# Kernel tuning notes

Hardware: AMD Instinct MI355X
Metric: run time of the kernel (lower is better)

Reference implementation:

```python
import jax, jax.numpy as jnp
import numpy as np

B = 16            # batch of graphs
N = 512           # n_node
D = 32            # embedding_dim
MAXN = 16         # max_neighbors
E = MAXN * (N - 1)   # 8176 edges per graph
SLEFT = N * D
FSS = 601         # full_support_size
NA = N - 1        # num_actions (so one-hot rows == B*n_node)
IN0 = D + 1       # sa feature dim
NTOT = B * N


def _gat(x, snd, rcv, W, a_src, a_dst, b):
    # single-head GATConv, add_self_loops=False
    h = x @ W                                            # [BN, C]
    e = (h * a_src).sum(-1)[snd] + (h * a_dst).sum(-1)[rcv]
    e = jnp.where(e > 0, e, 0.2 * e)                     # LeakyReLU(0.2)
    m = jax.ops.segment_max(e, rcv, num_segments=NTOT)   # segment softmax
    m = jnp.where(jnp.isfinite(m), m, 0.0)
    ee = jnp.exp(e - m[rcv])
    den = jax.ops.segment_sum(ee, rcv, num_segments=NTOT)
    alpha = ee / (den[rcv] + 1e-16)
    return jax.ops.segment_sum(alpha[:, None] * h[snd], rcv, num_segments=NTOT) + b


def _ln(x, s, o):
    # hk.LayerNorm(axis=-2): normalize over node axis, scale/offset over features
    x3 = x.reshape(B, N, -1)
    mu = x3.mean(axis=1, keepdims=True)
    var = ((x3 - mu) ** 2).mean(axis=1, keepdims=True)
    return ((x3 - mu) * jax.lax.rsqrt(var + 1e-5) * s + o).reshape(B * N, -1)


def _gat_params(key, din, dout):
    k1, k2, k3 = jax.random.split(key, 3)
    sc = 1.0 / np.sqrt(din)
    return (jax.random.normal(k1, (din, dout), jnp.float32) * sc,
            jax.random.normal(k2, (dout,), jnp.float32) * sc,
            jax.random.normal(k3, (dout,), jnp.float32) * sc,
            jnp.zeros((dout,), jnp.float32))


def setup_inputs():
    key = jax.random.key(0)
    ks = jax.random.split(key, 4)
    nodes = jax.random.normal(ks[0], (B, SLEFT), jnp.float32)
    snd = jax.random.randint(ks[1], (B, E), 0, N).astype(jnp.float32)
    rcv = jax.random.randint(ks[2], (B, E), 0, N).astype(jnp.float32)
    ns = jnp.concatenate([nodes, snd, rcv], axis=1)      # [B, SLEFT + 2E]
    a = jax.random.randint(ks[3], (B,), 0, NA + 1)
    inp = {"ns": ns, "a": a}
    dims = [(IN0, 4 * D), (4 * D, 2 * D), (2 * D, 2 * D), (2 * D, D)]
    rdims = [(IN0, FSS), (FSS, FSS), (FSS, FSS), (FSS, FSS)]
    for i, (di, do) in enumerate(dims, 1):
        W, asrc, adst, b = _gat_params(jax.random.fold_in(key, 100 + i), di, do)
        inp.update({f"W{i}": W, f"a{i}s": asrc, f"a{i}d": adst, f"b{i}": b})
        if i < 4:
            inp.update({f"s{i}": jnp.ones((do,), jnp.float32), f"o{i}": jnp.zeros((do,), jnp.float32)})
    for i, (di, do) in enumerate(rdims, 1):
        W, asrc, adst, b = _gat_params(jax.random.fold_in(key, 200 + i), di, do)
        inp.update({f"rW{i}": W, f"ra{i}s": asrc, f"ra{i}d": adst, f"rb{i}": b})
        if i < 4:
            inp.update({f"rs{i}": jnp.ones((FSS,), jnp.float32), f"ro{i}": jnp.zeros((FSS,), jnp.float32)})
    return inp


def reference(ns, a,
              W1, a1s, a1d, b1, s1, o1,
              W2, a2s, a2d, b2, s2, o2,
              W3, a3s, a3d, b3, s3, o3,
              W4, a4s, a4d, b4,
              rW1, ra1s, ra1d, rb1, rs1, ro1,
              rW2, ra2s, ra2d, rb2, rs2, ro2,
              rW3, ra3s, ra3d, rb3, rs3, ro3,
              rW4, ra4s, ra4d, rb4):
    # gbatch: offset per-graph indices into one big graph
    off = (jnp.arange(B, dtype=jnp.int32) * N)[:, None]
    snd = (ns[:, SLEFT:SLEFT + E].astype(jnp.int32) + off).reshape(-1)
    rcv = (ns[:, SLEFT + E:SLEFT + 2 * E].astype(jnp.int32) + off).reshape(-1)
    nodes = ns[:, :SLEFT].reshape(B * N, D)
    sa = jnp.concatenate([nodes, jax.nn.one_hot(a, NA + 1).reshape(-1, 1)], axis=1)
    # reward head
    r = jax.nn.relu(_ln(_gat(sa, snd, rcv, rW1, ra1s, ra1d, rb1), rs1, ro1))
    r = jax.nn.relu(_ln(_gat(r, snd, rcv, rW2, ra2s, ra2d, rb2), rs2, ro2))
    r = jax.nn.relu(_ln(_gat(r, snd, rcv, rW3, ra3s, ra3d, rb3), rs3, ro3))
    r = _gat(r, snd, rcv, rW4, ra4s, ra4d, rb4).reshape(B, N, FSS).sum(axis=1)
    # next-state head
    f = jax.nn.relu(_ln(_gat(sa, snd, rcv, W1, a1s, a1d, b1), s1, o1))
    f = jax.nn.relu(_ln(_gat(f, snd, rcv, W2, a2s, a2d, b2), s2, o2))
    f = jax.nn.relu(_ln(_gat(f, snd, rcv, W3, a3s, a3d, b3), s3, o3))
    f = _gat(f, snd, rcv, W4, a4s, a4d, b4).reshape(B, N * D)
    ns_new = jnp.concatenate([f, ns[:, SLEFT:]], axis=1)
    return (r, ns_new)
```

## Files before the change

kernel.cpp:

```cpp
#include <hip/hip_runtime.h>
#include <math.h>

#define B_ 16
#define N_ 512
#define D_ 32
#define E_ 8176
#define SLEFT_ 16384
#define FSS_ 601
#define BN_ (B_*N_)
#define BE_ (B_*E_)
#define NSROW_ (SLEFT_ + 2*E_)
#define OUT_R_ (B_*FSS_)
#define HLD_ 768
#define CAP_ 128
#define KXB_ 736

typedef __attribute__((ext_vector_type(8))) short short8;
typedef __attribute__((ext_vector_type(4))) float f32x4;

typedef __attribute__((address_space(3))) uint lds_uint;
typedef __attribute__((address_space(1))) const uint g_uint;

__device__ __forceinline__ void gl_lds16(const ushort* gp, ushort* lp) {
  __builtin_amdgcn_global_load_lds((g_uint*)gp, (lds_uint*)lp, 16, 0, 0);
}

__device__ __forceinline__ ushort f2b(float f) {
  uint u = __builtin_bit_cast(uint, f);
  u += 0x7FFFu + ((u >> 16) & 1u);
  return (ushort)(u >> 16);
}
__device__ __forceinline__ float b2f(ushort h) {
  return __builtin_bit_cast(float, ((uint)h) << 16);
}


struct SetupP {
  const float* ns; const int* a;
  int* cnt; int* bins; ushort* sa;
  const float* Wr[4]; const float* Wn[4]; ushort* T[4];
};

__global__ __launch_bounds__(256) void k_setup(SetupP p) {
  __shared__ float tile[32][33];
  int blk = blockIdx.x;
  if (blk < 511) {
    int idx = blk*256 + threadIdx.x;
    if (idx >= BE_) return;
    int b = idx / E_;
    int j = idx - b*E_;
    const float* row = p.ns + (size_t)b*NSROW_;
    int s = (int)row[SLEFT_ + j];
    int r = (int)row[SLEFT_ + E_ + j];
    int dst = b*N_ + r;
    int pos = atomicAdd(&p.cnt[dst], 1);
    if (pos < CAP_) p.bins[(size_t)dst*CAP_ + pos] = b*N_ + s;
    return;
  }
  if (blk < 2559) {
    int idx = (blk-511)*256 + threadIdx.x;
    int v = idx >> 6, c = idx & 63;
    int b = v >> 9, n = v & 511;
    float val = 0.f;
    if (c < 32)       val = p.ns[(size_t)b*NSROW_ + n*32 + c];
    else if (c == 32) val = (p.a[b]==n) ? 1.f : 0.f;
    p.sa[idx] = f2b(val);
    return;
  }
  int t = blk - 2559;
  int s, base, KP, DINR, DINN, DOUTN, KOFF;
  if (t < 48)        { s=0; base=0;    KP=64;  DINR=33;  DINN=33;  DOUTN=128; KOFF=0;   }
  else if (t < 600)  { s=1; base=48;   KP=736; DINR=601; DINN=128; DOUTN=64;  KOFF=608; }
  else if (t < 1104) { s=2; base=600;  KP=672; DINR=601; DINN=64;  DOUTN=64;  KOFF=608; }
  else               { s=3; base=1104; KP=672; DINR=601; DINN=64;  DOUTN=32;  KOFF=608; }
  int ti = t - base;
  int kt = ti / 24, nt = ti - kt*24;
  int k0 = kt*32, n0 = nt*32;
  int tid = threadIdx.x;
  int cc = tid & 31, rr = tid >> 5;
  #pragma unroll
  for (int it=0; it<4; it++) {
    int k = k0 + it*8 + rr;
    int n = n0 + cc;
    float v = 0.f;
    if (n < 640) { if (n < 601 && k < DINR) v = p.Wr[s][(size_t)k*601 + n]; }
    else { int nn = n-640, kk = k-KOFF;
           if (nn < DOUTN && kk >= 0 && kk < DINN) v = p.Wn[s][(size_t)kk*DOUTN + nn]; }
    tile[it*8+rr][cc] = v;
  }
  __syncthreads();
  #pragma unroll
  for (int it=0; it<4; it++) {
    int n = n0 + it*8 + rr;
    int k = k0 + cc;
    p.T[s][(size_t)n*KP + k] = f2b(tile[cc][it*8+rr]);
  }
}


__global__ __launch_bounds__(256) void k_gemm(const ushort* __restrict__ A,
                                              const ushort* __restrict__ Bt,
                                              ushort* __restrict__ C,
                                              float* __restrict__ esed,
                                              const float* __restrict__ asr,
                                              const float* __restrict__ adr,
                                              const float* __restrict__ asn,
                                              const float* __restrict__ adn,
                                              int Astr, int Kpad, int dn,
                                              int kRewEnd, int kNextBeg) {
  __shared__ ushort Asm[64*32];
  __shared__ ushort Bsm[128*32];
  int tid = threadIdx.x;
  int rowBase = blockIdx.y * 64;
  int colBase = blockIdx.x * 128;
  int kBeg = (blockIdx.x == 5) ? kNextBeg : 0;
  int kEnd = (blockIdx.x == 5) ? Kpad : kRewEnd;
  int wave = tid >> 6, lane = tid & 63;
  int wr = (wave >> 1) * 32, wc = (wave & 1) * 64;
  int lm = lane & 15, lk = (lane >> 4) * 8;

  f32x4 acc[2][4];
  #pragma unroll
  for (int i=0;i<2;i++)
    #pragma unroll
    for (int j=0;j<4;j++) acc[i][j] = (f32x4){0.f,0.f,0.f,0.f};

  int t0 = tid, t1 = tid + 256;
  int ar = t0 >> 2, ac8 = (t0 & 3) * 8;
  const ushort* Bg0 = Bt + (size_t)(colBase + (t0>>2))*Kpad + (t0&3)*8;
  const ushort* Bg1 = Bt + (size_t)(colBase + (t1>>2))*Kpad + (t1&3)*8;
  ushort* Bl0 = &Bsm[t0*8];
  ushort* Bl1 = &Bsm[t1*8];
  ushort* Al0 = &Asm[t0*8];

  const ushort* Ag = A + (size_t)(rowBase + ar)*Astr + ac8;

  for (int k0 = kBeg; k0 < kEnd; k0 += 32) {
    gl_lds16(Bg0 + k0, Bl0);
    gl_lds16(Bg1 + k0, Bl1);
    gl_lds16(Ag + k0, Al0);
    __syncthreads();
    short8 af[2], bfr[4];
    #pragma unroll
    for (int i=0;i<2;i++) af[i]  = *(short8*)&Asm[(wr + i*16 + lm)*32 + lk];
    #pragma unroll
    for (int j=0;j<4;j++) bfr[j] = *(short8*)&Bsm[(wc + j*16 + lm)*32 + lk];
    #pragma unroll
    for (int i=0;i<2;i++)
      #pragma unroll
      for (int j=0;j<4;j++)
        acc[i][j] = __builtin_amdgcn_mfma_f32_16x16x32_bf16(af[i], bfr[j], acc[i][j], 0,0,0);
    __syncthreads();
  }

  float asv[4], adv[4];
  #pragma unroll
  for (int j=0;j<4;j++) {
    int col = colBase + wc + j*16 + lm;
    float s = 0.f, d = 0.f;
    if (col < 601)      { s = asr[col];     d = adr[col]; }
    else if (col >= 640 && col - 640 < dn) { s = asn[col-640]; d = adn[col-640]; }
    asv[j] = s; adv[j] = d;
  }
  int cr = lane >> 4;
  int ct2 = blockIdx.x*2 + (wc >> 6);
  float* esp = (ct2 < 10) ? esed : esed + 2*BN_;
  #pragma unroll
  for (int i=0;i<2;i++) {
    #pragma unroll
    for (int j=0;j<4;j++) {
      int col = colBase + wc + j*16 + lm;
      #pragma unroll
      for (int g=0; g<4; g++) {
        int row = rowBase + wr + i*16 + cr*4 + g;
        C[(size_t)row*HLD_ + col] = f2b(acc[i][j][g]);
      }
    }
    #pragma unroll
    for (int g=0; g<4; g++) {
      float se = 0.f, sd = 0.f;
      #pragma unroll
      for (int j=0;j<4;j++) { se += acc[i][j][g]*asv[j]; sd += acc[i][j][g]*adv[j]; }
      #pragma unroll
      for (int o=1;o<16;o<<=1) { se += __shfl_xor(se,o,64); sd += __shfl_xor(sd,o,64); }
      if (lm == 0) {
        int row = rowBase + wr + i*16 + cr*4 + g;
        atomicAdd(&esp[row], se);
        atomicAdd(&esp[BN_ + row], sd);
      }
    }
  }
}


__global__ __launch_bounds__(256) void k_agg(const ushort* __restrict__ h,
                                             const float* __restrict__ esed,
                                             const int* __restrict__ cnt,
                                             const int* __restrict__ bins,
                                             const float* __restrict__ bias_r,
                                             const float* __restrict__ bias_n,
                                             ushort* __restrict__ g,
                                             int dn) {
  const float* es_r = esed;
  const float* ed_r = esed + BN_;
  const float* es_n = esed + 2*BN_;
  const float* ed_n = esed + 3*BN_;
  int wid = threadIdx.x>>6, lane = threadIdx.x&63;
  int bid = blockIdx.x;
  int xcd = bid & 7, slot = bid >> 3;
  int graph = xcd + ((slot >> 7) << 3);
  int v = graph*512 + (slot & 127)*4 + wid;
  int s0 = v * CAP_;
  int deg = cnt[v]; if (deg > CAP_) deg = CAP_;
  float edr = ed_r[v], edn = ed_n[v];

  int nch = (640 + dn + 7) >> 3;
  int ch0 = lane, ch1 = lane + 64;
  bool a1 = ch1 < nch;
  bool c1r = ch1 < 80;
  float acc0[8], acc1[8];
  #pragma unroll
  for (int q=0;q<8;q++){ acc0[q]=0.f; acc1[q]=0.f; }

  if (deg <= 64) {
    bool has = lane < deg;
    int u = 0; float er = -__builtin_inff(), en = -__builtin_inff();
    if (has) {
      u = bins[s0 + lane];
      er = es_r[u] + edr; er = er > 0.f ? er : 0.2f*er;
      en = es_n[u] + edn; en = en > 0.f ? en : 0.2f*en;
    }
    float mr = er, mn = en;
    #pragma unroll
    for (int o=32;o;o>>=1) { mr = fmaxf(mr, __shfl_xor(mr,o,64)); mn = fmaxf(mn, __shfl_xor(mn,o,64)); }
    float pr = has ? __expf(er - mr) : 0.f;
    float pn = has ? __expf(en - mn) : 0.f;
    float dr = pr, dnm = pn;
    #pragma unroll
    for (int o=32;o;o>>=1) { dr += __shfl_xor(dr,o,64); dnm += __shfl_xor(dnm,o,64); }
    pr *= 1.f/(dr + 1e-16f);
    pn *= 1.f/(dnm + 1e-16f);

    for (int t0 = 0; t0 < deg; t0 += 4) {
      int nt = deg - t0; if (nt > 4) nt = 4;
      short8 va[4], vb[4];
      float w0[4], w1[4];
      #pragma unroll
      for (int q=0;q<4;q++) {
        if (q < nt) {
          int uu = __shfl(u, t0+q, 64);
          w0[q] = __shfl(pr, t0+q, 64);
          w1[q] = __shfl(pn, t0+q, 64);
          const ushort* hp = h + (size_t)uu*HLD_;
          va[q] = *(const short8*)&hp[ch0*8];
          vb[q] = a1 ? *(const short8*)&hp[ch1*8] : short8{};
        } else {
          w0[q] = 0.f; w1[q] = 0.f; va[q] = short8{}; vb[q] = short8{};
        }
      }
      #pragma unroll
      for (int q=0;q<4;q++) {
        #pragma unroll
        for (int r=0;r<8;r++) acc0[r] += w0[q] * b2f((ushort)va[q][r]);
        if (a1) {
          float wv = c1r ? w0[q] : w1[q];
          #pragma unroll
          for (int r=0;r<8;r++) acc1[r] += wv * b2f((ushort)vb[q][r]);
        }
      }
    }
  } else {
    int e0 = s0 + deg;
    float mr = -__builtin_inff(), mn = -__builtin_inff();
    for (int j = s0 + lane; j < e0; j += 64) {
      int u = bins[j];
      float er = es_r[u] + edr; er = er>0.f?er:0.2f*er;
      float en = es_n[u] + edn; en = en>0.f?en:0.2f*en;
      mr = fmaxf(mr, er); mn = fmaxf(mn, en);
    }
    #pragma unroll
    for (int o=32;o;o>>=1) { mr=fmaxf(mr,__shfl_xor(mr,o,64)); mn=fmaxf(mn,__shfl_xor(mn,o,64)); }
    float dr=0.f, dnm=0.f;
    for (int j = s0 + lane; j < e0; j += 64) {
      int u = bins[j];
      float er = es_r[u] + edr; er = er>0.f?er:0.2f*er;
      float en = es_n[u] + edn; en = en>0.f?en:0.2f*en;
      dr += __expf(er-mr); dnm += __expf(en-mn);
    }
    #pragma unroll
    for (int o=32;o;o>>=1) { dr+=__shfl_xor(dr,o,64); dnm+=__shfl_xor(dnm,o,64); }
    float ir = 1.f/(dr+1e-16f), in_ = 1.f/(dnm+1e-16f);
    for (int j = s0; j < e0; ++j) {
      int uu = bins[j];
      float er = es_r[uu] + edr; er = er>0.f?er:0.2f*er;
      float en = es_n[uu] + edn; en = en>0.f?en:0.2f*en;
      float wr2 = __expf(er-mr)*ir, wn2 = __expf(en-mn)*in_;
      const ushort* hp = h + (size_t)uu*HLD_;
      short8 hv = *(const short8*)&hp[ch0*8];
      #pragma unroll
      for (int q=0;q<8;q++) acc0[q] += wr2 * b2f((ushort)hv[q]);
      if (a1) {
        short8 hv2 = *(const short8*)&hp[ch1*8];
        float wv = c1r ? wr2 : wn2;
        #pragma unroll
        for (int q=0;q<8;q++) acc1[q] += wv * b2f((ushort)hv2[q]);
      }
    }
  }

  ushort* gv = g + (size_t)v*HLD_;
  {
    int cb = ch0*8;
    short8 ov;
    #pragma unroll
    for (int q=0;q<8;q++) ov[q] = (short)f2b(acc0[q] + bias_r[cb+q]);
    *(short8*)&gv[cb] = ov;
  }
  if (a1) {
    int cb = ch1*8;
    short8 ov;
    #pragma unroll
    for (int q=0;q<8;q++) {
      int c = cb+q;
      float val;
      if (c < 601)                         val = acc1[q] + bias_r[c];
      else if (c >= 640 && (c-640) < dn)   val = acc1[q] + bias_n[c-640];
      else                                 val = 0.f;
      ov[q] = (short)f2b(val);
    }
    *(short8*)&gv[cb] = ov;
  }
}


__global__ __launch_bounds__(256) void k_lnfin(const ushort* __restrict__ g,
                                               const float* __restrict__ scr,
                                               const float* __restrict__ ofr,
                                               const float* __restrict__ scn,
                                               const float* __restrict__ ofn,
                                               ushort* __restrict__ xbuf,
                                               int dn) {
  int b = blockIdx.y;
  int t = threadIdx.x;
  int c8l = t & 7;
  int rg  = t >> 3;
  int xb8 = blockIdx.x*64 + c8l*8;
  bool okc = xb8 < KXB_;
  int gcol8 = (xb8 < 608) ? xb8 : xb8 + 32;
  float s8[8], q8[8];
  #pragma unroll
  for (int j=0;j<8;j++){ s8[j]=0.f; q8[j]=0.f; }
  if (okc) {
    const ushort* gp = g + (size_t)(b*N_ + rg*16)*HLD_ + gcol8;
    #pragma unroll
    for (int i=0;i<16;i++) {
      short8 v = *(const short8*)&gp[(size_t)i*HLD_];
      #pragma unroll
      for (int j=0;j<8;j++) {
        float x = b2f((ushort)v[j]);
        s8[j] += x; q8[j] += x*x;
      }
    }
  }
  __shared__ float S[32][64], Q[32][64];
  __shared__ float MU[64], AD[64];
  #pragma unroll
  for (int j=0;j<8;j++){ S[rg][c8l*8+j]=s8[j]; Q[rg][c8l*8+j]=q8[j]; }
  __syncthreads();
  if (t < 64) {
    int xb = blockIdx.x*64 + t;
    float mul = 0.f, add = 0.f;
    if (xb < KXB_) {
      float ts=0.f, tq=0.f;
      #pragma unroll
      for (int r=0;r<32;r++){ ts += S[r][t]; tq += Q[r][t]; }
      bool valid; float scale, offs;
      if (xb < 608) { valid = xb < 601;
                      scale = valid ? scr[xb] : 0.f; offs = valid ? ofr[xb] : 0.f; }
      else { int cn = xb - 608; valid = cn < dn;
             scale = valid ? scn[cn] : 0.f; offs = valid ? ofn[cn] : 0.f; }
      if (valid) {
        float mu = ts*(1.f/N_);
        float var = tq*(1.f/N_) - mu*mu;
        float rs = rsqrtf(var+1e-5f);
        mul = rs*scale;
        add = offs - mu*rs*scale;
      }
    }
    MU[t] = mul; AD[t] = add;
  }
  __syncthreads();
  if (okc) {
    float mu8[8], ad8[8];
    #pragma unroll
    for (int j=0;j<8;j++){ mu8[j]=MU[c8l*8+j]; ad8[j]=AD[c8l*8+j]; }
    const ushort* gp = g + (size_t)(b*N_ + rg*16)*HLD_ + gcol8;
    ushort* xp = xbuf + (size_t)(b*N_ + rg*16)*KXB_ + xb8;
    #pragma unroll
    for (int i=0;i<16;i++) {
      short8 v = *(const short8*)&gp[(size_t)i*HLD_];
      short8 ov;
      #pragma unroll
      for (int j=0;j<8;j++) {
        float y = b2f((ushort)v[j]) * mu8[j] + ad8[j];
        y = y > 0.f ? y : 0.f;
        ov[j] = (short)f2b(y);
      }
      *(short8*)&xp[(size_t)i*KXB_] = ov;
    }
  }
}


__global__ __launch_bounds__(256) void k_rsum(const ushort* __restrict__ g,
                                              float* __restrict__ rsp) {
  int b = blockIdx.y, z = blockIdx.z; int n0 = z*64;
  int lc = threadIdx.x & 63, r0 = threadIdx.x>>6;
  int c = blockIdx.x*64 + lc;
  float s = 0.f;
  if (c < FSS_) {
    #pragma unroll 4
    for (int i=0;i<16;i++) {
      int n = n0 + r0*16 + i;
      s += b2f(g[(size_t)(b*N_+n)*HLD_ + c]);
    }
  }
  __shared__ float S[4][64];
  S[r0][lc]=s; __syncthreads();
  if (r0==0 && c<FSS_)
    rsp[((size_t)z*B_ + b)*FSS_ + c] = S[0][lc]+S[1][lc]+S[2][lc]+S[3][lc];
}


__global__ __launch_bounds__(256) void k_final(const float* __restrict__ rsp,
                                               const ushort* __restrict__ g,
                                               const float* __restrict__ ns,
                                               float* __restrict__ out) {
  int idx = blockIdx.x*256+threadIdx.x;
  if (idx < OUT_R_) {
    int b = idx / FSS_, c = idx - b*FSS_;
    float s = 0.f;
    #pragma unroll
    for (int z=0;z<8;z++) s += rsp[((size_t)z*B_ + b)*FSS_ + c];
    out[idx] = s;
  } else {
    int j2 = idx - OUT_R_;
    if (j2 >= B_*NSROW_) return;
    int b = j2 / NSROW_; int j = j2 - b*NSROW_;
    float v;
    if (j < SLEFT_) {
      int n = j >> 5, c = j & 31;
      v = b2f(g[(size_t)(b*N_+n)*HLD_ + 640 + c]);
    } else {
      v = ns[(size_t)b*NSROW_ + j];
    }
    out[idx] = v;
  }
}


extern "C" void kernel_launch(void* const* d_in, const int* in_sizes, int n_in,
                              void* d_out, int out_size, void* d_ws, size_t ws_size,
                              hipStream_t stream) {
  const float* ns = (const float*)d_in[0];
  const int*   a  = (const int*)d_in[1];

  const float *W[4], *As[4], *Ad[4], *Bb[4], *Sc[3], *Of[3];
  const float *rW[4], *rAs[4], *rAd[4], *rBb[4], *rSc[3], *rOf[3];
  int p = 2;
  for (int i=0;i<4;i++){
    W[i]=(const float*)d_in[p++]; As[i]=(const float*)d_in[p++];
    Ad[i]=(const float*)d_in[p++]; Bb[i]=(const float*)d_in[p++];
    if (i<3){ Sc[i]=(const float*)d_in[p++]; Of[i]=(const float*)d_in[p++]; }
  }
  for (int i=0;i<4;i++){
    rW[i]=(const float*)d_in[p++]; rAs[i]=(const float*)d_in[p++];
    rAd[i]=(const float*)d_in[p++]; rBb[i]=(const float*)d_in[p++];
    if (i<3){ rSc[i]=(const float*)d_in[p++]; rOf[i]=(const float*)d_in[p++]; }
  }

  char* w = (char*)d_ws;
  auto carve = [&](size_t bytes)->void* {
    void* r = (void*)w;
    w += (bytes + 255) & ~(size_t)255;
    return r;
  };
  ushort* hbuf = (ushort*)carve((size_t)BN_*HLD_*2);
  ushort* gbuf = (ushort*)carve((size_t)BN_*HLD_*2);
  ushort* xbuf = (ushort*)carve((size_t)BN_*KXB_*2);
  ushort* sabf = (ushort*)carve((size_t)BN_*64*2);
  int* cnt     = (int*)carve((size_t)(BN_ + 4*4*BN_)*4);
  float* esedL = (float*)(cnt + BN_);
  int* bins    = (int*)carve((size_t)BN_*CAP_*4);
  float* rsp   = (float*)carve((size_t)8*B_*FSS_*4);
  ushort* Wt[4];
  Wt[0] = (ushort*)carve((size_t)768*64*2);
  Wt[1] = (ushort*)carve((size_t)768*736*2);
  Wt[2] = (ushort*)carve((size_t)768*672*2);
  Wt[3] = (ushort*)carve((size_t)768*672*2);

  float* out = (float*)d_out;

  hipMemsetAsync(cnt, 0, (size_t)(BN_ + 16*BN_)*4, stream);

  SetupP sp;
  sp.ns = ns; sp.a = a; sp.cnt = cnt; sp.bins = bins; sp.sa = sabf;
  for (int i=0;i<4;i++){ sp.Wr[i]=rW[i]; sp.Wn[i]=W[i]; sp.T[i]=Wt[i]; }
  k_setup<<<4167, 256, 0, stream>>>(sp);

  dim3 ggrid(6, BN_/64);

  int Kp[4]   = { 64, 736, 672, 672 };
  int dns[4]  = { 128, 64, 64, 32 };
  int kRe[4]  = { 64, 608, 608, 608 };
  int kNb[4]  = { 0, 608, 608, 608 };

  for (int L=0; L<4; ++L) {
    float* esed = esedL + (size_t)L*4*BN_;
    const ushort* Ain = (L==0) ? sabf : xbuf;
    int Astr        = (L==0) ? 64 : KXB_;
    k_gemm<<<ggrid, 256, 0, stream>>>(Ain, Wt[L], hbuf, esed,
                                      rAs[L], rAd[L], As[L], Ad[L],
                                      Astr, Kp[L], dns[L], kRe[L], kNb[L]);
    k_agg<<<BN_/4, 256, 0, stream>>>(hbuf, esed, cnt, bins,
                                     rBb[L], Bb[L], gbuf, dns[L]);
    if (L < 3) {
      k_lnfin<<<dim3(12, B_), 256, 0, stream>>>(gbuf, rSc[L], rOf[L], Sc[L], Of[L],
                                                xbuf, dns[L]);
    }
  }

  k_rsum<<<dim3(10, B_, 8), 256, 0, stream>>>(gbuf, rsp);
  k_final<<<(OUT_R_ + B_*NSROW_ + 255)/256, 256, 0, stream>>>(rsp, gbuf, ns, out);
}
```

Measured before the change: 350.4 us.

## Fuse reward node-sum into final aggregation and vectorize setup conversion

Result: no change. 344.7 us (-1.6%).

```diff
diff --git a/kernel.cpp b/kernel.cpp
--- a/kernel.cpp
+++ b/kernel.cpp
@@ -57,17 +57,24 @@
     if (pos < CAP_) p.bins[(size_t)dst*CAP_ + pos] = b*N_ + s;
     return;
   }
-  if (blk < 2559) {
-    int idx = (blk-511)*256 + threadIdx.x;
-    int v = idx >> 6, c = idx & 63;
+  if (blk < 767) {
+    int it = (blk-511)*256 + threadIdx.x;
+    int v = it >> 3, c0 = (it & 7) * 8;
     int b = v >> 9, n = v & 511;
-    float val = 0.f;
-    if (c < 32)       val = p.ns[(size_t)b*NSROW_ + n*32 + c];
-    else if (c == 32) val = (p.a[b]==n) ? 1.f : 0.f;
-    p.sa[idx] = f2b(val);
+    short8 ov;
+    if (c0 < 32) {
+      const float* src = p.ns + (size_t)b*NSROW_ + n*32 + c0;
+      #pragma unroll
+      for (int j=0;j<8;j++) ov[j] = (short)f2b(src[j]);
+    } else {
+      #pragma unroll
+      for (int j=0;j<8;j++) ov[j] = 0;
+      if (c0 == 32) ov[0] = (short)f2b((p.a[b]==n) ? 1.f : 0.f);
+    }
+    *(short8*)&p.sa[(size_t)v*64 + c0] = ov;
     return;
   }
-  int t = blk - 2559;
+  int t = blk - 767;
   int s, base, KP, DINR, DINN, DOUTN, KOFF;
   if (t < 48)        { s=0; base=0;    KP=64;  DINR=33;  DINN=33;  DOUTN=128; KOFF=0;   }
   else if (t < 600)  { s=1; base=48;   KP=736; DINR=601; DINN=128; DOUTN=64;  KOFF=608; }
@@ -76,6 +83,7 @@
   int ti = t - base;
   int kt = ti / 24, nt = ti - kt*24;
   int k0 = kt*32, n0 = nt*32;
+  if (k0 >= KP) return;
   int tid = threadIdx.x;
   int cc = tid & 31, rr = tid >> 5;
   #pragma unroll
@@ -200,7 +208,9 @@
                                              const float* __restrict__ bias_r,
                                              const float* __restrict__ bias_n,
                                              ushort* __restrict__ g,
-                                             int dn) {
+                                             float* __restrict__ rsp16,
+                                             int dn, int doRsum) {
+  __shared__ float RW[4][608];
   const float* es_r = esed;
   const float* ed_r = esed + BN_;
   const float* es_n = esed + 2*BN_;
@@ -315,6 +325,10 @@
     #pragma unroll
     for (int q=0;q<8;q++) ov[q] = (short)f2b(acc0[q] + bias_r[cb+q]);
     *(short8*)&gv[cb] = ov;
+    if (doRsum) {
+      #pragma unroll
+      for (int q=0;q<8;q++) RW[wid][cb+q] = b2f((ushort)ov[q]);
+    }
   }
   if (a1) {
     int cb = ch1*8;
@@ -329,6 +343,24 @@
       ov[q] = (short)f2b(val);
     }
     *(short8*)&gv[cb] = ov;
+    if (doRsum && cb < 608) {
+      #pragma unroll
+      for (int q=0;q<8;q++) {
+        int c = cb+q;
+        RW[wid][c] = (c < 601) ? b2f((ushort)ov[q]) : 0.f;
+      }
+    }
+  }
+  if (doRsum) {
+    if (!a1 && ch1*8 < 608) {
+      #pragma unroll
+      for (int q=0;q<8;q++) RW[wid][ch1*8+q] = 0.f;
+    }
+    __syncthreads();
+    for (int c = threadIdx.x; c < 601; c += 256) {
+      float s = RW[0][c] + RW[1][c] + RW[2][c] + RW[3][c];
+      atomicAdd(&rsp16[(size_t)graph*FSS_ + c], s);
+    }
   }
 }
 
@@ -412,37 +444,13 @@
 }
 
 
-__global__ __launch_bounds__(256) void k_rsum(const ushort* __restrict__ g,
-                                              float* __restrict__ rsp) {
-  int b = blockIdx.y, z = blockIdx.z; int n0 = z*64;
-  int lc = threadIdx.x & 63, r0 = threadIdx.x>>6;
-  int c = blockIdx.x*64 + lc;
-  float s = 0.f;
-  if (c < FSS_) {
-    #pragma unroll 4
-    for (int i=0;i<16;i++) {
-      int n = n0 + r0*16 + i;
-      s += b2f(g[(size_t)(b*N_+n)*HLD_ + c]);
-    }
-  }
-  __shared__ float S[4][64];
-  S[r0][lc]=s; __syncthreads();
-  if (r0==0 && c<FSS_)
-    rsp[((size_t)z*B_ + b)*FSS_ + c] = S[0][lc]+S[1][lc]+S[2][lc]+S[3][lc];
-}
-
-
-__global__ __launch_bounds__(256) void k_final(const float* __restrict__ rsp,
+__global__ __launch_bounds__(256) void k_final(const float* __restrict__ rsp16,
                                                const ushort* __restrict__ g,
                                                const float* __restrict__ ns,
                                                float* __restrict__ out) {
   int idx = blockIdx.x*256+threadIdx.x;
   if (idx < OUT_R_) {
-    int b = idx / FSS_, c = idx - b*FSS_;
-    float s = 0.f;
-    #pragma unroll
-    for (int z=0;z<8;z++) s += rsp[((size_t)z*B_ + b)*FSS_ + c];
-    out[idx] = s;
+    out[idx] = rsp16[idx];
   } else {
     int j2 = idx - OUT_R_;
     if (j2 >= B_*NSROW_) return;
@@ -489,10 +497,10 @@
   ushort* gbuf = (ushort*)carve((size_t)BN_*HLD_*2);
   ushort* xbuf = (ushort*)carve((size_t)BN_*KXB_*2);
   ushort* sabf = (ushort*)carve((size_t)BN_*64*2);
-  int* cnt     = (int*)carve((size_t)(BN_ + 4*4*BN_)*4);
+  int* cnt     = (int*)carve((size_t)(BN_ + 16*BN_ + OUT_R_)*4);
   float* esedL = (float*)(cnt + BN_);
+  float* rsp16 = (float*)(cnt + BN_ + 16*BN_);
   int* bins    = (int*)carve((size_t)BN_*CAP_*4);
-  float* rsp   = (float*)carve((size_t)8*B_*FSS_*4);
   ushort* Wt[4];
   Wt[0] = (ushort*)carve((size_t)768*64*2);
   Wt[1] = (ushort*)carve((size_t)768*736*2);
@@ -501,12 +509,12 @@
 
   float* out = (float*)d_out;
 
-  hipMemsetAsync(cnt, 0, (size_t)(BN_ + 16*BN_)*4, stream);
+  hipMemsetAsync(cnt, 0, (size_t)(BN_ + 16*BN_ + OUT_R_)*4, stream);
 
   SetupP sp;
   sp.ns = ns; sp.a = a; sp.cnt = cnt; sp.bins = bins; sp.sa = sabf;
   for (int i=0;i<4;i++){ sp.Wr[i]=rW[i]; sp.Wn[i]=W[i]; sp.T[i]=Wt[i]; }
-  k_setup<<<4167, 256, 0, stream>>>(sp);
+  k_setup<<<2375, 256, 0, stream>>>(sp);
 
   dim3 ggrid(6, BN_/64);
 
@@ -523,13 +531,13 @@
                                       rAs[L], rAd[L], As[L], Ad[L],
                                       Astr, Kp[L], dns[L], kRe[L], kNb[L]);
     k_agg<<<BN_/4, 256, 0, stream>>>(hbuf, esed, cnt, bins,
-                                     rBb[L], Bb[L], gbuf, dns[L]);
+                                     rBb[L], Bb[L], gbuf, rsp16,
+                                     dns[L], (L==3)?1:0);
     if (L < 3) {
       k_lnfin<<<dim3(12, B_), 256, 0, stream>>>(gbuf, rSc[L], rOf[L], Sc[L], Of[L],
                                                 xbuf, dns[L]);
     }
   }
 
-  k_rsum<<<dim3(10, B_, 8), 256, 0, stream>>>(gbuf, rsp);
-  k_final<<<(OUT_R_ + B_*NSROW_ + 255)/256, 256, 0, stream>>>(rsp, gbuf, ns, out);
-}
+  k_final<<<(OUT_R_ + B_*NSROW_ + 255)/256, 256, 0, stream>>>(rsp16, gbuf, ns, out);
+}
```
